# Kernel optimization log

Measured on AMD Instinct MI355X. Metric: run time of the kernel, lower is better.

## Reference

```python
import jax, jax.numpy as jnp
import numpy as np

RANKS = [384, 320, 256, 256, 192, 192, 128, 128]
NUM_GROUPS = len(RANKS)
IN_FEATURES = 4096
OUT_FEATURES = 4096
GROUP_DIM = OUT_FEATURES // NUM_GROUPS  # 512
NUM_HEADS = 32
HEAD_DIM = OUT_FEATURES // NUM_HEADS  # 128
INVERSE_INDICES = np.array([26, 1, 19, 0, 11, 25, 18, 2, 13, 3, 30, 4, 5, 29, 12, 6, 16, 7, 20, 8, 27, 9, 10, 14, 31, 15, 23, 17, 21, 22, 24, 28], dtype=np.int32)
BATCH, SEQ = 4, 4096


def setup_inputs() -> dict:
    key = jax.random.key(0)
    ks = jax.random.split(key, 2 + 2 * NUM_GROUPS)
    inp = {
        "hidden_states": jax.random.normal(ks[0], (BATCH, SEQ, IN_FEATURES), dtype=jnp.float32) * 0.02,
        "VT_w": jax.random.normal(ks[1], (sum(RANKS), IN_FEATURES), dtype=jnp.float32) * 0.02,
    }
    for i, r in enumerate(RANKS):
        inp[f"U_w{i}"] = jax.random.normal(ks[2 + 2 * i], (GROUP_DIM, r), dtype=jnp.float32) * 0.02
        inp[f"U_b{i}"] = jax.random.normal(ks[3 + 2 * i], (GROUP_DIM,), dtype=jnp.float32) * 0.02
    return inp


def reference(hidden_states, VT_w,
              U_w0, U_w1, U_w2, U_w3, U_w4, U_w5, U_w6, U_w7,
              U_b0, U_b1, U_b2, U_b3, U_b4, U_b5, U_b6, U_b7):
    Uw = [U_w0, U_w1, U_w2, U_w3, U_w4, U_w5, U_w6, U_w7]
    Ub = [U_b0, U_b1, U_b2, U_b3, U_b4, U_b5, U_b6, U_b7]
    # project_to_latent: one big GEMM -> [B, L, sum(ranks)]
    latents = jnp.einsum('bld,rd->blr', hidden_states, VT_w)
    # reconstruct: per-group small GEMMs (num_groups is small and ranks differ)
    outs = []
    offset = 0
    for i, r in enumerate(RANKS):
        out_i = jnp.einsum('blr,gr->blg', latents[..., offset:offset + r], Uw[i]) + Ub[i]
        outs.append(out_i)
        offset += r
    output = jnp.concatenate(outs, axis=-1)  # [B, L, OUT_FEATURES]
    # inverse head reorder
    B, L, D = output.shape
    output = output.reshape(B, L, NUM_HEADS, HEAD_DIM)
    output = output[:, :, jnp.asarray(INVERSE_INDICES), :]
    return output.reshape(B, L, D)
```

## Files before the change

### kernel.cpp

```cpp
#include <hip/hip_runtime.h>
#include <stdint.h>

typedef unsigned short u16;
typedef __attribute__((ext_vector_type(8))) __bf16 bf16x8;
typedef __attribute__((ext_vector_type(4))) float f32x4;

#define M_TOT   16384
#define K1      4096
#define N1_PAD  1920
#define N1_REAL 1856

__constant__ int c_FWD[32] = {3,1,7,9,11,12,15,17,19,21,22,4,14,8,23,25,
                              16,27,6,2,18,28,29,26,30,5,0,20,31,13,10,24};
__constant__ int c_OFF[8]  = {0,384,704,960,1216,1408,1600,1728};
__constant__ int c_RANK[8] = {384,320,256,256,192,192,128,128};

__device__ __forceinline__ u16 f2bf(float x) {
  unsigned int u = __builtin_bit_cast(unsigned int, x);
  u += 0x7fffu + ((u >> 16) & 1u);
  return (u16)(u >> 16);
}

__device__ __forceinline__ void gload_lds16(const u16* g, u16* l) {
  __builtin_amdgcn_global_load_lds(
      (const __attribute__((address_space(1))) unsigned int*)g,
      (__attribute__((address_space(3))) unsigned int*)l, 16, 0, 0);
}

__global__ void cvt_f32_bf16(const float* __restrict__ src, u16* __restrict__ dst, int n4) {
  int i = blockIdx.x * blockDim.x + threadIdx.x;
  if (i >= n4) return;
  float4 v = reinterpret_cast<const float4*>(src)[i];
  uint64_t pack = (uint64_t)f2bf(v.x) | ((uint64_t)f2bf(v.y) << 16) |
                  ((uint64_t)f2bf(v.z) << 32) | ((uint64_t)f2bf(v.w) << 48);
  reinterpret_cast<uint64_t*>(dst)[i] = pack;
}

__global__ void cvt_pad_vt(const float* __restrict__ src, u16* __restrict__ dst) {
  int i = blockIdx.x * blockDim.x + threadIdx.x;
  if (i >= (N1_PAD * K1 / 4)) return;
  int row = i >> 10;
  uint64_t pack = 0;
  if (row < N1_REAL) {
    float4 v = reinterpret_cast<const float4*>(src)[i];
    pack = (uint64_t)f2bf(v.x) | ((uint64_t)f2bf(v.y) << 16) |
           ((uint64_t)f2bf(v.z) << 32) | ((uint64_t)f2bf(v.w) << 48);
  }
  reinterpret_cast<uint64_t*>(dst)[i] = pack;
}

struct GroupPtrs { const float* uw[8]; const float* ub[8]; };

__global__ void pack_u_bias(GroupPtrs gp, u16* __restrict__ ub, float* __restrict__ bias) {
  const int g = blockIdx.y;
  const int rank = c_RANK[g];
  const int n4 = (512 * rank) >> 2;
  const int idx = blockIdx.x * blockDim.x + threadIdx.x;
  if (idx < n4) {
    float4 v = reinterpret_cast<const float4*>(gp.uw[g])[idx];
    uint64_t pack = (uint64_t)f2bf(v.x) | ((uint64_t)f2bf(v.y) << 16) |
                    ((uint64_t)f2bf(v.z) << 32) | ((uint64_t)f2bf(v.w) << 48);
    reinterpret_cast<uint64_t*>(ub + (size_t)512 * c_OFF[g])[idx] = pack;
  }
  if (blockIdx.x == 0 && idx < 128) {
    reinterpret_cast<float4*>(bias + (g << 9))[idx] =
        reinterpret_cast<const float4*>(gp.ub[g])[idx];
  }
}

__global__ void gemm1_kernel(const u16* __restrict__ A, const u16* __restrict__ B,
                             u16* __restrict__ C) {
  __shared__ u16 lA[128 * 64];
  __shared__ u16 lB[128 * 64];
  const int tid  = threadIdx.x;
  const int wave = tid >> 6, lane = tid & 63;
  const int lr = lane & 15, lk = lane >> 4;
  const int wm = wave >> 1, wn = wave & 1;

  const int W   = blockIdx.x;
  const int xcd = W & 7, idx = W >> 3;
  const int mt  = (idx / 15) + xcd * 16;
  const int nt  = idx % 15;
  const int row0 = mt * 128;
  const int col0 = nt * 128;

  const u16* Ab = A + (size_t)row0 * K1;
  const u16* Bb = B + (size_t)col0 * K1;

  f32x4 acc[4][4] = {};

  for (int kt = 0; kt < K1 / 64; ++kt) {
    __syncthreads();
#pragma unroll
    for (int q = 0; q < 4; ++q) {
      int ci = q * 256 + tid;
      int r = ci >> 3, c = ci & 7;
      int ldst = (q * 256 + wave * 64) * 8;
      gload_lds16(Ab + (size_t)r * K1 + kt * 64 + c * 8, lA + ldst);
      gload_lds16(Bb + (size_t)r * K1 + kt * 64 + c * 8, lB + ldst);
    }
    __syncthreads();
#pragma unroll
    for (int kk = 0; kk < 2; ++kk) {
      bf16x8 af[4], bfr[4];
#pragma unroll
      for (int m = 0; m < 4; ++m)
        af[m] = *reinterpret_cast<const bf16x8*>(&lA[(wm * 64 + m * 16 + lr) * 64 + kk * 32 + lk * 8]);
#pragma unroll
      for (int n = 0; n < 4; ++n)
        bfr[n] = *reinterpret_cast<const bf16x8*>(&lB[(wn * 64 + n * 16 + lr) * 64 + kk * 32 + lk * 8]);
#pragma unroll
      for (int m = 0; m < 4; ++m)
#pragma unroll
        for (int n = 0; n < 4; ++n)
          acc[m][n] = __builtin_amdgcn_mfma_f32_16x16x32_bf16(af[m], bfr[n], acc[m][n], 0, 0, 0);
    }
  }

#pragma unroll
  for (int n = 0; n < 4; ++n) {
    int col = col0 + wn * 64 + n * 16 + lr;
#pragma unroll
    for (int m = 0; m < 4; ++m) {
#pragma unroll
      for (int v = 0; v < 4; ++v) {
        int row = row0 + wm * 64 + m * 16 + lk * 4 + v;
        C[(size_t)row * N1_PAD + col] = f2bf(acc[m][n][v]);
      }
    }
  }
}

__global__ void gemm2_kernel(const u16* __restrict__ A,
                             const u16* __restrict__ Uall,
                             const float* __restrict__ bias,
                             float* __restrict__ out) {
  const int tid  = threadIdx.x;
  const int wave = tid >> 6, lane = tid & 63;
  const int lr = lane & 15, lk = lane >> 4;
  const int wm = wave >> 1, wn = wave & 1;

  const int W   = blockIdx.x;
  const int xcd = W & 7, idx = W >> 3;
  const int mt  = (idx >> 5) + xcd * 16;
  const int rem = idx & 31;
  const int g   = rem >> 2;
  const int nt  = rem & 3;

  const int rank = c_RANK[g], off = c_OFF[g];
  __shared__ u16 lA[128 * 64];
  __shared__ u16 lB[128 * 64];
  const int row0 = mt * 128;
  const int col0 = nt * 128;

  const u16* Ab = A + (size_t)row0 * N1_PAD + off;
  const u16* Bb = Uall + (size_t)512 * off + (size_t)col0 * rank;

  f32x4 acc[4][4] = {};

  const int nkt = rank >> 6;
  for (int kt = 0; kt < nkt; ++kt) {
    __syncthreads();
#pragma unroll
    for (int q = 0; q < 4; ++q) {
      int ci = q * 256 + tid;
      int r = ci >> 3, c = ci & 7;
      int ldst = (q * 256 + wave * 64) * 8;
      gload_lds16(Ab + (size_t)r * N1_PAD + kt * 64 + c * 8, lA + ldst);
      gload_lds16(Bb + (size_t)r * rank   + kt * 64 + c * 8, lB + ldst);
    }
    __syncthreads();
#pragma unroll
    for (int kk = 0; kk < 2; ++kk) {
      bf16x8 af[4], bfr[4];
#pragma unroll
      for (int m = 0; m < 4; ++m)
        af[m] = *reinterpret_cast<const bf16x8*>(&lA[(wm * 64 + m * 16 + lr) * 64 + kk * 32 + lk * 8]);
#pragma unroll
      for (int n = 0; n < 4; ++n)
        bfr[n] = *reinterpret_cast<const bf16x8*>(&lB[(wn * 64 + n * 16 + lr) * 64 + kk * 32 + lk * 8]);
#pragma unroll
      for (int m = 0; m < 4; ++m)
#pragma unroll
        for (int n = 0; n < 4; ++n)
          acc[m][n] = __builtin_amdgcn_mfma_f32_16x16x32_bf16(af[m], bfr[n], acc[m][n], 0, 0, 0);
    }
  }

#pragma unroll
  for (int n = 0; n < 4; ++n) {
    int cg = col0 + wn * 64 + n * 16 + lr;
    int h  = (g << 2) + (cg >> 7);
    int oc = (c_FWD[h] << 7) | (cg & 127);
    float bv = bias[(g << 9) + cg];
#pragma unroll
    for (int m = 0; m < 4; ++m) {
#pragma unroll
      for (int v = 0; v < 4; ++v) {
        int row = row0 + wm * 64 + m * 16 + lk * 4 + v;
        out[(size_t)row * 4096 + oc] = acc[m][n][v] + bv;
      }
    }
  }
}

extern "C" void kernel_launch(void* const* d_in, const int* in_sizes, int n_in,
                              void* d_out, int out_size, void* d_ws, size_t ws_size,
                              hipStream_t stream) {
  const float* hs = (const float*)d_in[0];
  const float* vt = (const float*)d_in[1];

  u16* hsb = (u16*)d_ws;
  u16* vtb = hsb + (size_t)M_TOT * K1;
  u16* lat = vtb + (size_t)N1_PAD * K1;
  u16* ub  = lat + (size_t)M_TOT * N1_PAD;
  float* bias = (float*)(ub + (size_t)512 * N1_REAL);

  {
    int n4 = M_TOT * K1 / 4;
    cvt_f32_bf16<<<n4 / 256, 256, 0, stream>>>(hs, hsb, n4);
  }
  {
    int n4 = N1_PAD * K1 / 4;
    cvt_pad_vt<<<(n4 + 255) / 256, 256, 0, stream>>>(vt, vtb);
  }
  {
    GroupPtrs gp;
    for (int g = 0; g < 8; ++g) {
      gp.uw[g] = (const float*)d_in[2 + 2 * g];
      gp.ub[g] = (const float*)d_in[3 + 2 * g];
    }
    pack_u_bias<<<dim3(192, 8), 256, 0, stream>>>(gp, ub, bias);
  }

  gemm1_kernel<<<dim3(1920), 256, 0, stream>>>(hsb, vtb, lat);

  gemm2_kernel<<<dim3(4096), 256, 0, stream>>>(lat, ub, bias, (float*)d_out);
}
```

Baseline: 838.7 us.

## Rewrite gemm2 as LDS-free per-wave 32x64 tiles reading directly from global

The second GEMM moves from 128x128 block tiles staged through shared memory with barriers to per-wave 32x64 output tiles. Each wave loads its MFMA fragments straight from global memory, which leaves the kernel with no LDS and no __syncthreads. The grid doubles to keep the GPU occupied with the smaller tiles. This removes barrier and LDS staging overhead, at the cost of lower data reuse per load, more redundant global and L2 reads, and fragment loads that are less well coalesced.

```diff
diff --git a/kernel.cpp b/kernel.cpp
--- a/kernel.cpp
+++ b/kernel.cpp
@@ -138,67 +138,51 @@
   const int tid  = threadIdx.x;
   const int wave = tid >> 6, lane = tid & 63;
   const int lr = lane & 15, lk = lane >> 4;
-  const int wm = wave >> 1, wn = wave & 1;
-
-  const int W   = blockIdx.x;
-  const int xcd = W & 7, idx = W >> 3;
-  const int mt  = (idx >> 5) + xcd * 16;
-  const int rem = idx & 31;
-  const int g   = rem >> 2;
-  const int nt  = rem & 3;
-
+
+  const int b   = blockIdx.x;
+  const int xcd = b & 7, i = b >> 3;
+  const int ms  = (i >> 4) + xcd * 64;
+  const int cs  = ((i & 15) << 2) + wave;
+
+  const int c0   = cs << 6;
+  const int g    = c0 >> 9;
+  const int cg0  = c0 & 511;
   const int rank = c_RANK[g], off = c_OFF[g];
-  __shared__ u16 lA[128 * 64];
-  __shared__ u16 lB[128 * 64];
-  const int row0 = mt * 128;
-  const int col0 = nt * 128;
+  const int h    = (g << 2) + (cg0 >> 7);
+  const int oc0  = (c_FWD[h] << 7) + (cg0 & 127);
+  const int row0 = ms << 5;
 
   const u16* Ab = A + (size_t)row0 * N1_PAD + off;
-  const u16* Bb = Uall + (size_t)512 * off + (size_t)col0 * rank;
-
-  f32x4 acc[4][4] = {};
-
-  const int nkt = rank >> 6;
-  for (int kt = 0; kt < nkt; ++kt) {
-    __syncthreads();
-#pragma unroll
-    for (int q = 0; q < 4; ++q) {
-      int ci = q * 256 + tid;
-      int r = ci >> 3, c = ci & 7;
-      int ldst = (q * 256 + wave * 64) * 8;
-      gload_lds16(Ab + (size_t)r * N1_PAD + kt * 64 + c * 8, lA + ldst);
-      gload_lds16(Bb + (size_t)r * rank   + kt * 64 + c * 8, lB + ldst);
-    }
-    __syncthreads();
-#pragma unroll
-    for (int kk = 0; kk < 2; ++kk) {
-      bf16x8 af[4], bfr[4];
-#pragma unroll
-      for (int m = 0; m < 4; ++m)
-        af[m] = *reinterpret_cast<const bf16x8*>(&lA[(wm * 64 + m * 16 + lr) * 64 + kk * 32 + lk * 8]);
+  const u16* Bb = Uall + (size_t)512 * off + (size_t)cg0 * rank;
+
+  f32x4 acc[2][4] = {};
+  const int nkk = rank >> 5;
+#pragma unroll 2
+  for (int kk = 0; kk < nkk; ++kk) {
+    bf16x8 af[2], bfr[4];
+#pragma unroll
+    for (int m = 0; m < 2; ++m)
+      af[m] = *reinterpret_cast<const bf16x8*>(&Ab[(size_t)(m * 16 + lr) * N1_PAD + kk * 32 + lk * 8]);
+#pragma unroll
+    for (int n = 0; n < 4; ++n)
+      bfr[n] = *reinterpret_cast<const bf16x8*>(&Bb[(size_t)(n * 16 + lr) * rank + kk * 32 + lk * 8]);
+#pragma unroll
+    for (int m = 0; m < 2; ++m)
 #pragma unroll
       for (int n = 0; n < 4; ++n)
-        bfr[n] = *reinterpret_cast<const bf16x8*>(&lB[(wn * 64 + n * 16 + lr) * 64 + kk * 32 + lk * 8]);
-#pragma unroll
-      for (int m = 0; m < 4; ++m)
-#pragma unroll
-        for (int n = 0; n < 4; ++n)
-          acc[m][n] = __builtin_amdgcn_mfma_f32_16x16x32_bf16(af[m], bfr[n], acc[m][n], 0, 0, 0);
-    }
+        acc[m][n] = __builtin_amdgcn_mfma_f32_16x16x32_bf16(af[m], bfr[n], acc[m][n], 0, 0, 0);
   }
 
 #pragma unroll
   for (int n = 0; n < 4; ++n) {
-    int cg = col0 + wn * 64 + n * 16 + lr;
-    int h  = (g << 2) + (cg >> 7);
-    int oc = (c_FWD[h] << 7) | (cg & 127);
-    float bv = bias[(g << 9) + cg];
-#pragma unroll
-    for (int m = 0; m < 4; ++m) {
+    int col = oc0 + n * 16 + lr;
+    float bv = bias[(g << 9) + cg0 + n * 16 + lr];
+#pragma unroll
+    for (int m = 0; m < 2; ++m) {
 #pragma unroll
       for (int v = 0; v < 4; ++v) {
-        int row = row0 + wm * 64 + m * 16 + lk * 4 + v;
-        out[(size_t)row * 4096 + oc] = acc[m][n][v] + bv;
+        int row = row0 + m * 16 + lk * 4 + v;
+        out[(size_t)row * 4096 + col] = acc[m][n][v] + bv;
       }
     }
   }
@@ -235,5 +219,5 @@
 
   gemm1_kernel<<<dim3(1920), 256, 0, stream>>>(hsb, vtb, lat);
 
-  gemm2_kernel<<<dim3(4096), 256, 0, stream>>>(lat, ub, bias, (float*)d_out);
-}
+  gemm2_kernel<<<dim3(8192), 256, 0, stream>>>(lat, ub, bias, (float*)d_out);
+}
```

Result: slower. 930.9 us (+11.0%).
